# Optimization experiments

Hardware: AMD Instinct MI355X
Metric: run time of the kernel (lower is better)

## Reference

```python
import jax, jax.numpy as jnp
import numpy as np

B, T, D, K = 64, 512, 1024, 10
TEMP = 0.07
EPS = 1e-8


def setup_inputs() -> dict:
    key = jax.random.key(0)
    features = jax.random.normal(key, (B, T, D), dtype=jnp.float32)
    # Replicate torch.randperm-based negative sampling: for each batch b,
    # sample K indices without replacement from the (B-1)*T vectors of all
    # other batches, then map flat index -> (batch, time).
    rng = np.random.default_rng(0)
    neg_b = np.empty((B, K), dtype=np.int64)
    neg_t = np.empty((B, K), dtype=np.int64)
    for b in range(B):
        idx = rng.permutation((B - 1) * T)[:K]
        bb = idx // T
        bb = bb + (bb >= b)  # skip own batch
        neg_b[b] = bb
        neg_t[b] = idx % T
    return {"features": features, "neg_b": jnp.asarray(neg_b), "neg_t": jnp.asarray(neg_t)}


def _unit(x):
    # torch F.cosine_similarity semantics: divide by max(||x||, eps)
    n = jnp.sqrt(jnp.sum(x * x, axis=-1, keepdims=True))
    return x / jnp.maximum(n, EPS)


def reference(features, neg_b, neg_t):
    anchors = features[:, 1:T - 1, :]     # [B, T-2, D]
    positives = features[:, 2:T, :]       # [B, T-2, D]
    a_hat = _unit(anchors)
    pos_sim = jnp.sum(a_hat * _unit(positives), axis=-1) / TEMP          # [B, T-2]
    negs = jax.lax.stop_gradient(features)[neg_b, neg_t]                  # [B, K, D]
    sim_neg = jnp.einsum('btd,bkd->btk', a_hat, _unit(negs)) / TEMP       # [B, T-2, K]
    exp_pos = jnp.exp(pos_sim)
    exp_neg = jnp.exp(sim_neg).sum(axis=-1)
    loss = -jnp.log(exp_pos / (exp_pos + exp_neg))                        # [B, T-2]
    return loss.mean(axis=1).mean()
```

## Files before the change

### kernel.cpp

```cpp
#include <hip/hip_runtime.h>

#define B_ 64
#define T_ 512
#define D_ 1024
#define K_ 10
constexpr float TEMP_ = 0.07f;
constexpr float EPS_ = 1e-8f;
constexpr int CHUNK = 32;
constexpr int NCHUNK = 16;
constexpr int F4ROW = D_ / 4;

__device__ __forceinline__ float dot4(float4 a, float4 b) {
    return a.x * b.x + a.y * b.y + a.z * b.z + a.w * b.w;
}

#if __has_builtin(__builtin_amdgcn_update_dpp)
template <int CTRL>
__device__ __forceinline__ float dpp_add(float x) {
    int y = __builtin_amdgcn_update_dpp(0, __float_as_int(x), CTRL, 0xf, 0xf, false);
    return x + __int_as_float(y);
}
__device__ __forceinline__ float red16(float x) {
    x = dpp_add<0x128>(x);
    x = dpp_add<0x124>(x);
    x = dpp_add<0x122>(x);
    x = dpp_add<0x121>(x);
    return x;
}
#else
__device__ __forceinline__ float red16(float x) {
    x += __shfl_xor(x, 8, 16);
    x += __shfl_xor(x, 4, 16);
    x += __shfl_xor(x, 2, 16);
    x += __shfl_xor(x, 1, 16);
    return x;
}
#endif

__global__ __launch_bounds__(256) void signcl_main(
    const float* __restrict__ features,
    const int* __restrict__ neg_b,
    const int* __restrict__ neg_t,
    float* __restrict__ partials)
{
    __shared__ float s_negs[K_ * D_];
    __shared__ float s_inv[K_];
    __shared__ float s_part[16];

    const int bid = blockIdx.x;
    const int b = bid >> 4;
    const int c = bid & (NCHUNK - 1);
    const int tid = threadIdx.x;

    const float4* f4 = reinterpret_cast<const float4*>(features);
    float4* s4 = reinterpret_cast<float4*>(s_negs);

#pragma unroll
    for (int it = 0; it < 10; ++it) {
        int idx = tid + it * 256;
        int k = idx >> 8;
        int off = idx & 255;
        int nb = neg_b[b * K_ + k];
        int nt = neg_t[b * K_ + k];
        s4[idx] = f4[((size_t)nb * T_ + nt) * F4ROW + off];
    }
    __syncthreads();

    const int lane = tid & 63;
    const int w = tid >> 6;
    for (int k = w; k < K_; k += 4) {
        float ss = 0.f;
#pragma unroll
        for (int s = 0; s < 4; ++s) {
            float4 v = s4[k * F4ROW + s * 64 + lane];
            ss += dot4(v, v);
        }
#pragma unroll
        for (int m = 32; m >= 1; m >>= 1) ss += __shfl_xor(ss, m, 64);
        if (lane == 0) s_inv[k] = 1.f / fmaxf(sqrtf(ss), EPS_);
    }
    __syncthreads();

#pragma unroll
    for (int it = 0; it < 10; ++it) {
        int idx = tid + it * 256;
        float inv = s_inv[idx >> 8];
        float4 v = s4[idx];
        v.x *= inv; v.y *= inv; v.z *= inv; v.w *= inv;
        s4[idx] = v;
    }
    __syncthreads();

    const int t0 = 1 + c * CHUNK;
    const int t1 = min(t0 + CHUNK, T_ - 1);
    const int g = lane >> 4;
    const int i = lane & 15;
    const int ta = t0 + w * 8 + 2 * g;

    const size_t rowbase = (size_t)b * T_ * F4ROW;
    const float4* p0 = f4 + rowbase + (size_t)min(ta,     T_ - 1) * F4ROW;
    const float4* p1 = f4 + rowbase + (size_t)min(ta + 1, T_ - 1) * F4ROW;
    const float4* p2 = f4 + rowbase + (size_t)min(ta + 2, T_ - 1) * F4ROW;

    float ss0 = 0.f, ss1 = 0.f, ss2 = 0.f, dp01 = 0.f, dp12 = 0.f;
    float nd0[K_], nd1[K_];
#pragma unroll
    for (int k = 0; k < K_; ++k) { nd0[k] = 0.f; nd1[k] = 0.f; }

#pragma unroll 4
    for (int s = 0; s < 16; ++s) {
        int fi = s * 16 + i;
        float4 a = p0[fi];
        float4 p = p1[fi];
        float4 q = p2[fi];
        ss0  += dot4(a, a);
        ss1  += dot4(p, p);
        ss2  += dot4(q, q);
        dp01 += dot4(a, p);
        dp12 += dot4(p, q);
#pragma unroll
        for (int k = 0; k < K_; ++k) {
            float4 n = s4[k * F4ROW + fi];
            nd0[k] += dot4(a, n);
            nd1[k] += dot4(p, n);
        }
    }

    ss0 = red16(ss0); ss1 = red16(ss1); ss2 = red16(ss2);
    dp01 = red16(dp01); dp12 = red16(dp12);
#pragma unroll
    for (int k = 0; k < K_; ++k) { nd0[k] = red16(nd0[k]); nd1[k] = red16(nd1[k]); }

    const float invT = 1.f / TEMP_;
    const float inv0 = 1.f / fmaxf(sqrtf(ss0), EPS_);
    const float inv1 = 1.f / fmaxf(sqrtf(ss1), EPS_);
    const float inv2 = 1.f / fmaxf(sqrtf(ss2), EPS_);

    float lsum = 0.f;
    if (ta < t1) {
        float pos = dp01 * inv0 * inv1 * invT;
        float se = 0.f;
#pragma unroll
        for (int k = 0; k < K_; ++k) se += __expf(nd0[k] * inv0 * invT);
        lsum += __logf(__expf(pos) + se) - pos;
    }
    if (ta + 1 < t1) {
        float pos = dp12 * inv1 * inv2 * invT;
        float se = 0.f;
#pragma unroll
        for (int k = 0; k < K_; ++k) se += __expf(nd1[k] * inv1 * invT);
        lsum += __logf(__expf(pos) + se) - pos;
    }

    if (i == 0) s_part[w * 4 + g] = lsum;
    __syncthreads();
    if (tid == 0) {
        float t = 0.f;
#pragma unroll
        for (int j = 0; j < 16; ++j) t += s_part[j];
        partials[bid] = t;
    }
}

__global__ __launch_bounds__(256) void signcl_reduce(
    const float* __restrict__ partials, float* __restrict__ out)
{
    __shared__ float s_w[4];
    const int tid = threadIdx.x;
    float s = 0.f;
    for (int idx = tid; idx < B_ * NCHUNK; idx += 256) s += partials[idx];
#pragma unroll
    for (int m = 32; m >= 1; m >>= 1) s += __shfl_xor(s, m, 64);
    const int w = tid >> 6, lane = tid & 63;
    if (lane == 0) s_w[w] = s;
    __syncthreads();
    if (tid == 0) {
        float t = s_w[0] + s_w[1] + s_w[2] + s_w[3];
        out[0] = t / (float)(B_ * (T_ - 2));
    }
}

extern "C" void kernel_launch(void* const* d_in, const int* in_sizes, int n_in,
                              void* d_out, int out_size, void* d_ws, size_t ws_size,
                              hipStream_t stream) {
    const float* features = (const float*)d_in[0];
    const int* neg_b = (const int*)d_in[1];
    const int* neg_t = (const int*)d_in[2];
    float* partials = (float*)d_ws;

    signcl_main<<<B_ * NCHUNK, 256, 0, stream>>>(features, neg_b, neg_t, partials);
    signcl_reduce<<<1, 256, 0, stream>>>(partials, (float*)d_out);
}
```

Measured before the change: 48.79 us.

## Store negatives as bf16 in LDS, halve chunk size, widen lane groups

Packs the gathered negative vectors into bf16 in shared memory, halving LDS footprint and read traffic, and sets a higher occupancy hint. The time chunk per block is halved to double the block count, and each pair of rows is now handled by 32 lanes using 8-wide loads with a DPP plus swizzle reduction. The cost is bf16 rounding error on the negatives and more redundant gathering of negatives and halo rows across blocks.

New measurement: 46.35 us. 5.0% less time.

```diff
diff --git a/kernel.cpp b/kernel.cpp
--- a/kernel.cpp
+++ b/kernel.cpp
@@ -6,55 +6,56 @@
 #define K_ 10
 constexpr float TEMP_ = 0.07f;
 constexpr float EPS_ = 1e-8f;
-constexpr int CHUNK = 32;
-constexpr int NCHUNK = 16;
+constexpr int CHUNK = 16;
+constexpr int NCHUNK = 32;
 constexpr int F4ROW = D_ / 4;
 
 __device__ __forceinline__ float dot4(float4 a, float4 b) {
     return a.x * b.x + a.y * b.y + a.z * b.z + a.w * b.w;
 }
 
-#if __has_builtin(__builtin_amdgcn_update_dpp)
+__device__ __forceinline__ unsigned bfr_(float f) {
+    unsigned u = __float_as_uint(f);
+    return (u + 0x7fffu + ((u >> 16) & 1u)) >> 16;
+}
+__device__ __forceinline__ unsigned pack2_(float lo, float hi) {
+    return bfr_(lo) | (bfr_(hi) << 16);
+}
+__device__ __forceinline__ float plo_(unsigned u) { return __uint_as_float(u << 16); }
+__device__ __forceinline__ float phi_(unsigned u) { return __uint_as_float(u & 0xffff0000u); }
+
 template <int CTRL>
 __device__ __forceinline__ float dpp_add(float x) {
     int y = __builtin_amdgcn_update_dpp(0, __float_as_int(x), CTRL, 0xf, 0xf, false);
     return x + __int_as_float(y);
 }
-__device__ __forceinline__ float red16(float x) {
+__device__ __forceinline__ float red32(float x) {
     x = dpp_add<0x128>(x);
     x = dpp_add<0x124>(x);
     x = dpp_add<0x122>(x);
     x = dpp_add<0x121>(x);
-    return x;
-}
-#else
-__device__ __forceinline__ float red16(float x) {
-    x += __shfl_xor(x, 8, 16);
-    x += __shfl_xor(x, 4, 16);
-    x += __shfl_xor(x, 2, 16);
-    x += __shfl_xor(x, 1, 16);
-    return x;
-}
-#endif
-
-__global__ __launch_bounds__(256) void signcl_main(
+    int y = __builtin_amdgcn_ds_swizzle(__float_as_int(x), 0x401F);
+    return x + __int_as_float(y);
+}
+
+__global__ __launch_bounds__(256, 7) void signcl_main(
     const float* __restrict__ features,
     const int* __restrict__ neg_b,
     const int* __restrict__ neg_t,
     float* __restrict__ partials)
 {
-    __shared__ float s_negs[K_ * D_];
+    __shared__ unsigned s_negs[K_ * 512];
     __shared__ float s_inv[K_];
-    __shared__ float s_part[16];
+    __shared__ float s_part[8];
 
     const int bid = blockIdx.x;
-    const int b = bid >> 4;
+    const int b = bid >> 5;
     const int c = bid & (NCHUNK - 1);
     const int tid = threadIdx.x;
 
     const float4* f4 = reinterpret_cast<const float4*>(features);
-    float4* s4 = reinterpret_cast<float4*>(s_negs);
-
+
+    uint2* s2 = reinterpret_cast<uint2*>(s_negs);
 #pragma unroll
     for (int it = 0; it < 10; ++it) {
         int idx = tid + it * 256;
@@ -62,18 +63,25 @@
         int off = idx & 255;
         int nb = neg_b[b * K_ + k];
         int nt = neg_t[b * K_ + k];
-        s4[idx] = f4[((size_t)nb * T_ + nt) * F4ROW + off];
+        float4 v = f4[((size_t)nb * T_ + nt) * F4ROW + off];
+        uint2 p;
+        p.x = pack2_(v.x, v.y);
+        p.y = pack2_(v.z, v.w);
+        s2[idx] = p;
     }
     __syncthreads();
 
     const int lane = tid & 63;
     const int w = tid >> 6;
     for (int k = w; k < K_; k += 4) {
+        const uint4* r4 = reinterpret_cast<const uint4*>(s_negs + k * 512);
         float ss = 0.f;
 #pragma unroll
-        for (int s = 0; s < 4; ++s) {
-            float4 v = s4[k * F4ROW + s * 64 + lane];
-            ss += dot4(v, v);
+        for (int j = 0; j < 2; ++j) {
+            uint4 u = r4[j * 64 + lane];
+            float e0 = plo_(u.x), e1 = phi_(u.x), e2 = plo_(u.y), e3 = phi_(u.y);
+            float e4 = plo_(u.z), e5 = phi_(u.z), e6 = plo_(u.w), e7 = phi_(u.w);
+            ss += e0*e0 + e1*e1 + e2*e2 + e3*e3 + e4*e4 + e5*e5 + e6*e6 + e7*e7;
         }
 #pragma unroll
         for (int m = 32; m >= 1; m >>= 1) ss += __shfl_xor(ss, m, 64);
@@ -81,21 +89,25 @@
     }
     __syncthreads();
 
-#pragma unroll
-    for (int it = 0; it < 10; ++it) {
-        int idx = tid + it * 256;
-        float inv = s_inv[idx >> 8];
-        float4 v = s4[idx];
-        v.x *= inv; v.y *= inv; v.z *= inv; v.w *= inv;
-        s4[idx] = v;
-    }
-    __syncthreads();
-
+    uint4* s4u = reinterpret_cast<uint4*>(s_negs);
+#pragma unroll
+    for (int j = 0; j < 5; ++j) {
+        int idx4 = tid + j * 256;
+        float inv = s_inv[idx4 >> 7];
+        uint4 u = s4u[idx4];
+        u.x = pack2_(plo_(u.x) * inv, phi_(u.x) * inv);
+        u.y = pack2_(plo_(u.y) * inv, phi_(u.y) * inv);
+        u.z = pack2_(plo_(u.z) * inv, phi_(u.z) * inv);
+        u.w = pack2_(plo_(u.w) * inv, phi_(u.w) * inv);
+        s4u[idx4] = u;
+    }
+    __syncthreads();
+
+    const int gid = tid >> 5;
+    const int i = tid & 31;
     const int t0 = 1 + c * CHUNK;
     const int t1 = min(t0 + CHUNK, T_ - 1);
-    const int g = lane >> 4;
-    const int i = lane & 15;
-    const int ta = t0 + w * 8 + 2 * g;
+    const int ta = t0 + gid * 2;
 
     const size_t rowbase = (size_t)b * T_ * F4ROW;
     const float4* p0 = f4 + rowbase + (size_t)min(ta,     T_ - 1) * F4ROW;
@@ -107,29 +119,34 @@
 #pragma unroll
     for (int k = 0; k < K_; ++k) { nd0[k] = 0.f; nd1[k] = 0.f; }
 
-#pragma unroll 4
-    for (int s = 0; s < 16; ++s) {
-        int fi = s * 16 + i;
-        float4 a = p0[fi];
-        float4 p = p1[fi];
-        float4 q = p2[fi];
-        ss0  += dot4(a, a);
-        ss1  += dot4(p, p);
-        ss2  += dot4(q, q);
-        dp01 += dot4(a, p);
-        dp12 += dot4(p, q);
+#pragma unroll
+    for (int s = 0; s < 4; ++s) {
+        int fi4 = s * 64 + i * 2;
+        float4 a0 = p0[fi4], a1 = p0[fi4 + 1];
+        float4 b0 = p1[fi4], b1 = p1[fi4 + 1];
+        float4 q0 = p2[fi4], q1 = p2[fi4 + 1];
+        ss0  += dot4(a0, a0) + dot4(a1, a1);
+        ss1  += dot4(b0, b0) + dot4(b1, b1);
+        ss2  += dot4(q0, q0) + dot4(q1, q1);
+        dp01 += dot4(a0, b0) + dot4(a1, b1);
+        dp12 += dot4(b0, q0) + dot4(b1, q1);
+        const uint4* nrow = reinterpret_cast<const uint4*>(s_negs) + s * 32 + i;
 #pragma unroll
         for (int k = 0; k < K_; ++k) {
-            float4 n = s4[k * F4ROW + fi];
-            nd0[k] += dot4(a, n);
-            nd1[k] += dot4(p, n);
+            uint4 u = nrow[k * 128];
+            float n0 = plo_(u.x), n1 = phi_(u.x), n2 = plo_(u.y), n3 = phi_(u.y);
+            float n4 = plo_(u.z), n5 = phi_(u.z), n6 = plo_(u.w), n7 = phi_(u.w);
+            nd0[k] += a0.x*n0 + a0.y*n1 + a0.z*n2 + a0.w*n3
+                    + a1.x*n4 + a1.y*n5 + a1.z*n6 + a1.w*n7;
+            nd1[k] += b0.x*n0 + b0.y*n1 + b0.z*n2 + b0.w*n3
+                    + b1.x*n4 + b1.y*n5 + b1.z*n6 + b1.w*n7;
         }
     }
 
-    ss0 = red16(ss0); ss1 = red16(ss1); ss2 = red16(ss2);
-    dp01 = red16(dp01); dp12 = red16(dp12);
-#pragma unroll
-    for (int k = 0; k < K_; ++k) { nd0[k] = red16(nd0[k]); nd1[k] = red16(nd1[k]); }
+    ss0 = red32(ss0); ss1 = red32(ss1); ss2 = red32(ss2);
+    dp01 = red32(dp01); dp12 = red32(dp12);
+#pragma unroll
+    for (int k = 0; k < K_; ++k) { nd0[k] = red32(nd0[k]); nd1[k] = red32(nd1[k]); }
 
     const float invT = 1.f / TEMP_;
     const float inv0 = 1.f / fmaxf(sqrtf(ss0), EPS_);
@@ -152,12 +169,12 @@
         lsum += __logf(__expf(pos) + se) - pos;
     }
 
-    if (i == 0) s_part[w * 4 + g] = lsum;
+    if (i == 0) s_part[gid] = lsum;
     __syncthreads();
     if (tid == 0) {
         float t = 0.f;
 #pragma unroll
-        for (int j = 0; j < 16; ++j) t += s_part[j];
+        for (int j = 0; j < 8; ++j) t += s_part[j];
         partials[bid] = t;
     }
 }
```
